# Performance work log

Hardware: AMD Instinct MI355X
Metric: run time of the kernel (lower is better)

The kernel has to match this reference:

```python
import jax, jax.numpy as jnp
import numpy as np

N_NODES = 100000
IN_DIM = 64
HIDDEN = 128
N_EDGES = 1600000


def sage_conv(x, src, dst, W_l, W_r, b):
    # PyG SAGEConv (mean aggr): out = lin_l(mean_{j in N(i)} x_j) + lin_r(x_i) + bias
    agg = jax.ops.segment_sum(x[src], dst, num_segments=N_NODES)  # [N, d]
    cnt = jax.ops.segment_sum(jnp.ones((src.shape[0],), x.dtype), dst,
                              num_segments=N_NODES)  # [N]
    mean = agg / jnp.maximum(cnt, 1.0)[:, None]
    return mean @ W_l + x @ W_r + b


def setup_inputs() -> dict:
    key = jax.random.key(0)
    ks = jax.random.split(key, 10)
    x = jax.random.normal(ks[0], (N_NODES, IN_DIM), dtype=jnp.float32)
    edge_index = jax.random.randint(ks[1], (2, N_EDGES), 0, N_NODES, dtype=jnp.int64)
    s = 1.0 / np.sqrt(IN_DIM)
    W_l1 = jax.random.uniform(ks[2], (IN_DIM, HIDDEN), jnp.float32, -s, s)
    W_r1 = jax.random.uniform(ks[3], (IN_DIM, HIDDEN), jnp.float32, -s, s)
    b1 = jnp.zeros((HIDDEN,), jnp.float32)
    s2 = 1.0 / np.sqrt(HIDDEN)
    W_l2 = jax.random.uniform(ks[4], (HIDDEN, HIDDEN), jnp.float32, -s2, s2)
    W_r2 = jax.random.uniform(ks[5], (HIDDEN, HIDDEN), jnp.float32, -s2, s2)
    b2 = jnp.zeros((HIDDEN,), jnp.float32)
    W_out = jax.random.uniform(ks[6], (HIDDEN, 1), jnp.float32, -s2, s2)
    b_out = jnp.zeros((1,), jnp.float32)
    return {"x": x, "edge_index": edge_index,
            "W_l1": W_l1, "W_r1": W_r1, "b1": b1,
            "W_l2": W_l2, "W_r2": W_r2, "b2": b2,
            "W_out": W_out, "b_out": b_out}


def reference(x, edge_index, W_l1, W_r1, b1, W_l2, W_r2, b2, W_out, b_out):
    src, dst = edge_index[0], edge_index[1]
    h1 = jax.nn.relu(sage_conv(x, src, dst, W_l1, W_r1, b1))   # [N, H]
    h2 = sage_conv(h1, src, dst, W_l2, W_r2, b2)               # [N, H]
    out = (h2 @ W_out + b_out).squeeze(-1)                     # [N]
    return out, h1, h2
```

## Files before the change

kernel.cpp:

```cpp
#include <hip/hip_runtime.h>

#define NN 100000
#define IND 64
#define HID 128
#define NE 1600000

#define BKT2 256
#define NBKT2 ((NN + BKT2 - 1) / BKT2)
#define CAP 4992
#define EPB 4096
#define NBLK_E ((NE + EPB - 1) / EPB)

#define CVT_BLKS (NN * IND / 4 / 256)
#define PW1_BLKS 8
#define PW2_BLKS 16

#define SCAN_CHUNK 1024
#define NSB ((NN + SCAN_CHUNK - 1) / SCAN_CHUNK)

typedef __attribute__((ext_vector_type(8))) short bf16x8;
typedef __attribute__((ext_vector_type(4))) float f32x4;
typedef __attribute__((ext_vector_type(2))) float f32x2;

static __device__ __forceinline__ unsigned short f2bf(float f) {
    unsigned u = __float_as_uint(f);
    u = (u + 0x7FFFu + ((u >> 16) & 1u)) >> 16;
    return (unsigned short)u;
}
static __device__ __forceinline__ unsigned pack2(float a, float b) {
    return (unsigned)f2bf(a) | ((unsigned)f2bf(b) << 16);
}


static __device__ __forceinline__ void packW_body(const float* __restrict__ Wr,
                                                  const float* __restrict__ Wl,
                                                  int Khalf, int KS, int t,
                                                  unsigned short* __restrict__ Wp) {
    if (t >= 8 * KS * 64) return;
    int l  = t & 63;
    int ks = (t >> 6) % KS;
    int jt = t / (64 * KS);
    int j  = jt * 16 + (l & 15);
    int kb = ks * 32 + (l >> 4) * 8;
    unsigned short v[8];
    #pragma unroll
    for (int i = 0; i < 8; ++i) {
        int k = kb + i;
        float w = (k < Khalf) ? Wr[k * HID + j] : Wl[(k - Khalf) * HID + j];
        v[i] = f2bf(w);
    }
    ushort4 lo, hi;
    lo.x = v[0]; lo.y = v[1]; lo.z = v[2]; lo.w = v[3];
    hi.x = v[4]; hi.y = v[5]; hi.z = v[6]; hi.w = v[7];
    ushort4* d = reinterpret_cast<ushort4*>(Wp + (size_t)t * 8);
    d[0] = lo; d[1] = hi;
}

__global__ __launch_bounds__(256) void prep_kernel(const float4* __restrict__ x,
                                                   unsigned* __restrict__ xq,
                                                   const float* __restrict__ Wr1,
                                                   const float* __restrict__ Wl1,
                                                   unsigned short* __restrict__ Wp1,
                                                   const float* __restrict__ Wr2,
                                                   const float* __restrict__ Wl2,
                                                   unsigned short* __restrict__ Wp2,
                                                   int* __restrict__ bktcur) {
    int blk = blockIdx.x, t = threadIdx.x;
    if (blk < CVT_BLKS) {
        int i = blk * 256 + t;
        float4 v = x[i];
        int u = __builtin_amdgcn_cvt_pk_fp8_f32(v.x, v.y, 0, false);
        u = __builtin_amdgcn_cvt_pk_fp8_f32(v.z, v.w, u, true);
        xq[i] = (unsigned)u;
    } else if (blk < CVT_BLKS + PW1_BLKS) {
        packW_body(Wr1, Wl1, IND, 4, (blk - CVT_BLKS) * 256 + t, Wp1);
    } else if (blk < CVT_BLKS + PW1_BLKS + PW2_BLKS) {
        packW_body(Wr2, Wl2, HID, 8, (blk - CVT_BLKS - PW1_BLKS) * 256 + t, Wp2);
    } else {
        bktcur[t] = 0;
        bktcur[t + 256] = 0;
    }
}


__global__ __launch_bounds__(512) void binA_kernel(const int* __restrict__ src,
                                                   const int* __restrict__ dst,
                                                   int* __restrict__ bktcur,
                                                   unsigned* __restrict__ bins) {
    __shared__ int hcnt[NBKT2];
    __shared__ int rbase[NBKT2];
    int t = threadIdx.x;
    int e0 = blockIdx.x * EPB;
    int ce = min(EPB, NE - e0);
    for (int i = t; i < NBKT2; i += 512) hcnt[i] = 0;
    __syncthreads();
    for (int i = t; i < ce; i += 512)
        atomicAdd(&hcnt[dst[e0 + i] >> 8], 1);
    __syncthreads();
    for (int i = t; i < NBKT2; i += 512) {
        int c = hcnt[i];
        rbase[i] = c ? atomicAdd(&bktcur[i], c) : 0;
        hcnt[i] = 0;
    }
    __syncthreads();
    for (int i = t; i < ce; i += 512) {
        int d = dst[e0 + i];
        int b = d >> 8;
        int r = atomicAdd(&hcnt[b], 1);
        bins[(size_t)b * CAP + rbase[b] + r] =
            (unsigned)src[e0 + i] | ((unsigned)(d & 255) << 17);
    }
}

__global__ __launch_bounds__(512) void binB_kernel(const int* __restrict__ bktcur,
                                                   unsigned* __restrict__ bins,
                                                   int* __restrict__ cnt,
                                                   int* __restrict__ off) {
    __shared__ unsigned ebuf[CAP];
    __shared__ int ncnt[BKT2];
    __shared__ int nofs[BKT2];
    __shared__ int wtot[4];
    int t = threadIdx.x, lane = t & 63, w = t >> 6;
    int b = blockIdx.x;
    int m = bktcur[b];
    size_t base = (size_t)b * CAP;
    for (int i = t; i < m; i += 512) ebuf[i] = bins[base + i];
    if (t < BKT2) ncnt[t] = 0;
    __syncthreads();
    for (int i = t; i < m; i += 512)
        atomicAdd(&ncnt[ebuf[i] >> 17], 1);
    __syncthreads();
    if (t < BKT2) {
        int v = ncnt[t];
        int incl = v;
        #pragma unroll
        for (int o = 1; o < 64; o <<= 1) {
            int u = __shfl_up(incl, o);
            if (lane >= o) incl += u;
        }
        if (lane == 63) wtot[w] = incl;
        nofs[t] = incl - v;
    }
    __syncthreads();
    if (t < BKT2) {
        int wbase = 0;
        #pragma unroll
        for (int i = 0; i < 4; ++i) if (i < w) wbase += wtot[i];
        int ex = nofs[t] + wbase;
        nofs[t] = ex;
        int node = b * BKT2 + t;
        if (node < NN) { cnt[node] = ncnt[t]; off[node] = (int)base + ex; }
    }
    __syncthreads();
    for (int i = t; i < m; i += 512) {
        unsigned val = ebuf[i];
        int r = atomicAdd(&nofs[val >> 17], 1);
        bins[base + r] = val & 0x1FFFFu;
    }
}


__global__ __launch_bounds__(256) void agg1_kernel(const unsigned char* __restrict__ xq,
                                                   const int* __restrict__ srcs,
                                                   const int* __restrict__ off,
                                                   const int* __restrict__ cnt,
                                                   unsigned short* __restrict__ m1b) {
    int t = threadIdx.x;
    int n = blockIdx.x * 4 + (t >> 6);
    int l = t & 63, ep = l >> 3, doff = (l & 7) * 8;
    int s0 = off[n], deg = cnt[n];
    float acc[8];
    #pragma unroll
    for (int i = 0; i < 8; ++i) acc[i] = 0.f;
    int e = ep;
    for (; e + 8 < deg; e += 16) {
        int sA = srcs[s0 + e], sB = srcs[s0 + e + 8];
        uint2 uA = *reinterpret_cast<const uint2*>(xq + (size_t)sA * IND + doff);
        uint2 uB = *reinterpret_cast<const uint2*>(xq + (size_t)sB * IND + doff);
        #pragma unroll
        for (int hw = 0; hw < 2; ++hw) {
            unsigned ua = hw ? uA.y : uA.x;
            unsigned ub = hw ? uB.y : uB.x;
            f32x2 la = __builtin_amdgcn_cvt_pk_f32_fp8((int)ua, false);
            f32x2 ha = __builtin_amdgcn_cvt_pk_f32_fp8((int)ua, true);
            f32x2 lb = __builtin_amdgcn_cvt_pk_f32_fp8((int)ub, false);
            f32x2 hb = __builtin_amdgcn_cvt_pk_f32_fp8((int)ub, true);
            acc[hw * 4 + 0] += la.x + lb.x;
            acc[hw * 4 + 1] += la.y + lb.y;
            acc[hw * 4 + 2] += ha.x + hb.x;
            acc[hw * 4 + 3] += ha.y + hb.y;
        }
    }
    for (; e < deg; e += 8) {
        int s = srcs[s0 + e];
        uint2 u = *reinterpret_cast<const uint2*>(xq + (size_t)s * IND + doff);
        #pragma unroll
        for (int hw = 0; hw < 2; ++hw) {
            unsigned uu = hw ? u.y : u.x;
            f32x2 lo = __builtin_amdgcn_cvt_pk_f32_fp8((int)uu, false);
            f32x2 hi = __builtin_amdgcn_cvt_pk_f32_fp8((int)uu, true);
            acc[hw * 4 + 0] += lo.x; acc[hw * 4 + 1] += lo.y;
            acc[hw * 4 + 2] += hi.x; acc[hw * 4 + 3] += hi.y;
        }
    }
    #pragma unroll
    for (int o = 8; o <= 32; o <<= 1) {
        #pragma unroll
        for (int i = 0; i < 8; ++i) acc[i] += __shfl_xor(acc[i], o);
    }
    if (l < 8) {
        float inv = 1.f / fmaxf((float)deg, 1.f);
        uint4 o;
        o.x = pack2(acc[0] * inv, acc[1] * inv);
        o.y = pack2(acc[2] * inv, acc[3] * inv);
        o.z = pack2(acc[4] * inv, acc[5] * inv);
        o.w = pack2(acc[6] * inv, acc[7] * inv);
        *reinterpret_cast<uint4*>(m1b + (size_t)n * IND + l * 8) = o;
    }
}

__global__ __launch_bounds__(256) void agg2_kernel(const unsigned char* __restrict__ h1q,
                                                   const int* __restrict__ srcs,
                                                   const int* __restrict__ off,
                                                   const int* __restrict__ cnt,
                                                   unsigned short* __restrict__ m2b) {
    int t = threadIdx.x;
    int n = blockIdx.x * 4 + (t >> 6);
    int l = t & 63, ep = l >> 3, doff = (l & 7) * 16;
    int s0 = off[n], deg = cnt[n];
    float acc[16];
    #pragma unroll
    for (int i = 0; i < 16; ++i) acc[i] = 0.f;
    int e = ep;
    for (; e + 8 < deg; e += 16) {
        int sA = srcs[s0 + e], sB = srcs[s0 + e + 8];
        uint4 uA = *reinterpret_cast<const uint4*>(h1q + (size_t)sA * HID + doff);
        uint4 uB = *reinterpret_cast<const uint4*>(h1q + (size_t)sB * HID + doff);
        unsigned wa[4] = {uA.x, uA.y, uA.z, uA.w};
        unsigned wb[4] = {uB.x, uB.y, uB.z, uB.w};
        #pragma unroll
        for (int q = 0; q < 4; ++q) {
            f32x2 la = __builtin_amdgcn_cvt_pk_f32_fp8((int)wa[q], false);
            f32x2 ha = __builtin_amdgcn_cvt_pk_f32_fp8((int)wa[q], true);
            f32x2 lb = __builtin_amdgcn_cvt_pk_f32_fp8((int)wb[q], false);
            f32x2 hb = __builtin_amdgcn_cvt_pk_f32_fp8((int)wb[q], true);
            acc[q * 4 + 0] += la.x + lb.x;
            acc[q * 4 + 1] += la.y + lb.y;
            acc[q * 4 + 2] += ha.x + hb.x;
            acc[q * 4 + 3] += ha.y + hb.y;
        }
    }
    for (; e < deg; e += 8) {
        int s = srcs[s0 + e];
        uint4 u = *reinterpret_cast<const uint4*>(h1q + (size_t)s * HID + doff);
        unsigned wu[4] = {u.x, u.y, u.z, u.w};
        #pragma unroll
        for (int q = 0; q < 4; ++q) {
            f32x2 lo = __builtin_amdgcn_cvt_pk_f32_fp8((int)wu[q], false);
            f32x2 hi = __builtin_amdgcn_cvt_pk_f32_fp8((int)wu[q], true);
            acc[q * 4 + 0] += lo.x; acc[q * 4 + 1] += lo.y;
            acc[q * 4 + 2] += hi.x; acc[q * 4 + 3] += hi.y;
        }
    }
    #pragma unroll
    for (int o = 8; o <= 32; o <<= 1) {
        #pragma unroll
        for (int i = 0; i < 16; ++i) acc[i] += __shfl_xor(acc[i], o);
    }
    if (l < 8) {
        float inv = 1.f / fmaxf((float)deg, 1.f);
        uint4 o1, o2;
        o1.x = pack2(acc[0] * inv,  acc[1] * inv);
        o1.y = pack2(acc[2] * inv,  acc[3] * inv);
        o1.z = pack2(acc[4] * inv,  acc[5] * inv);
        o1.w = pack2(acc[6] * inv,  acc[7] * inv);
        o2.x = pack2(acc[8] * inv,  acc[9] * inv);
        o2.y = pack2(acc[10] * inv, acc[11] * inv);
        o2.z = pack2(acc[12] * inv, acc[13] * inv);
        o2.w = pack2(acc[14] * inv, acc[15] * inv);
        unsigned short* dstp = m2b + (size_t)n * HID + l * 16;
        *reinterpret_cast<uint4*>(dstp) = o1;
        *reinterpret_cast<uint4*>(dstp + 8) = o2;
    }
}


__global__ __launch_bounds__(256) void mfma1_kernel(const float* __restrict__ x,
                                                    const unsigned short* __restrict__ m1b,
                                                    const unsigned short* __restrict__ Wp,
                                                    const float* __restrict__ b,
                                                    float* __restrict__ h1f,
                                                    unsigned short* __restrict__ h1b,
                                                    unsigned char* __restrict__ h1q) {
    int t = threadIdx.x, w = t >> 6, l = t & 63;
    int row0 = blockIdx.x * 64 + w * 16;
    int arow = row0 + (l & 15); if (arow > NN - 1) arow = NN - 1;
    int kcol = (l >> 4) * 8;
    f32x4 acc[8];
    #pragma unroll
    for (int jt = 0; jt < 8; ++jt) { acc[jt][0] = 0.f; acc[jt][1] = 0.f; acc[jt][2] = 0.f; acc[jt][3] = 0.f; }
    #pragma unroll
    for (int ks = 0; ks < 4; ++ks) {
        bf16x8 a;
        int c = (ks & 1) * 32 + kcol;
        if (ks < 2) {
            const float* xr = x + (size_t)arow * IND + c;
            float4 f0 = *reinterpret_cast<const float4*>(xr);
            float4 f1 = *reinterpret_cast<const float4*>(xr + 4);
            a[0] = (short)f2bf(f0.x); a[1] = (short)f2bf(f0.y);
            a[2] = (short)f2bf(f0.z); a[3] = (short)f2bf(f0.w);
            a[4] = (short)f2bf(f1.x); a[5] = (short)f2bf(f1.y);
            a[6] = (short)f2bf(f1.z); a[7] = (short)f2bf(f1.w);
        } else {
            a = *reinterpret_cast<const bf16x8*>(m1b + (size_t)arow * IND + c);
        }
        #pragma unroll
        for (int jt = 0; jt < 8; ++jt) {
            bf16x8 bb = *reinterpret_cast<const bf16x8*>(Wp + ((size_t)(jt * 4 + ks) * 64 + l) * 8);
            acc[jt] = __builtin_amdgcn_mfma_f32_16x16x32_bf16(a, bb, acc[jt], 0, 0, 0);
        }
    }
    int rbase = row0 + (l >> 4) * 4;
    #pragma unroll
    for (int jt = 0; jt < 8; ++jt) {
        int col = jt * 16 + (l & 15);
        float bias = b[col];
        #pragma unroll
        for (int r = 0; r < 4; ++r) {
            int row = rbase + r;
            if (row < NN) {
                float v = fmaxf(acc[jt][r] + bias, 0.f);
                h1f[(size_t)row * HID + col] = v;
                h1b[(size_t)row * HID + col] = f2bf(v);
                unsigned q8 = (unsigned)__builtin_amdgcn_cvt_pk_fp8_f32(v, 0.f, 0, false) & 0xFFu;
                h1q[(size_t)row * HID + col] = (unsigned char)q8;
            }
        }
    }
}

__global__ __launch_bounds__(256) void mfma2_kernel(const unsigned short* __restrict__ h1b,
                                                    const unsigned short* __restrict__ m2b,
                                                    const unsigned short* __restrict__ Wp,
                                                    const float* __restrict__ b,
                                                    const float* __restrict__ Wout,
                                                    const float* __restrict__ bout,
                                                    float* __restrict__ h2f,
                                                    float* __restrict__ out) {
    int t = threadIdx.x, w = t >> 6, l = t & 63;
    int row0 = blockIdx.x * 64 + w * 16;
    int arow = row0 + (l & 15); if (arow > NN - 1) arow = NN - 1;
    int kcol = (l >> 4) * 8;
    f32x4 acc[8];
    #pragma unroll
    for (int jt = 0; jt < 8; ++jt) { acc[jt][0] = 0.f; acc[jt][1] = 0.f; acc[jt][2] = 0.f; acc[jt][3] = 0.f; }
    #pragma unroll
    for (int ks = 0; ks < 8; ++ks) {
        const unsigned short* A = (ks < 4) ? h1b : m2b;
        int c = (ks & 3) * 32 + kcol;
        bf16x8 a = *reinterpret_cast<const bf16x8*>(A + (size_t)arow * HID + c);
        #pragma unroll
        for (int jt = 0; jt < 8; ++jt) {
            bf16x8 bb = *reinterpret_cast<const bf16x8*>(Wp + ((size_t)(jt * 8 + ks) * 64 + l) * 8);
            acc[jt] = __builtin_amdgcn_mfma_f32_16x16x32_bf16(a, bb, acc[jt], 0, 0, 0);
        }
    }
    int rbase = row0 + (l >> 4) * 4;
    float hs0 = 0.f, hs1 = 0.f, hs2 = 0.f, hs3 = 0.f;
    #pragma unroll
    for (int jt = 0; jt < 8; ++jt) {
        int col = jt * 16 + (l & 15);
        float bias = b[col];
        float wo = Wout[col];
        #pragma unroll
        for (int r = 0; r < 4; ++r) {
            int row = rbase + r;
            float v = acc[jt][r] + bias;
            if (row < NN) h2f[(size_t)row * HID + col] = v;
            if (r == 0) hs0 += v * wo;
            else if (r == 1) hs1 += v * wo;
            else if (r == 2) hs2 += v * wo;
            else hs3 += v * wo;
        }
    }
    #pragma unroll
    for (int o = 1; o < 16; o <<= 1) {
        hs0 += __shfl_xor(hs0, o);
        hs1 += __shfl_xor(hs1, o);
        hs2 += __shfl_xor(hs2, o);
        hs3 += __shfl_xor(hs3, o);
    }
    if ((l & 15) == 0) {
        float bo = bout[0];
        if (rbase + 0 < NN) out[rbase + 0] = hs0 + bo;
        if (rbase + 1 < NN) out[rbase + 1] = hs1 + bo;
        if (rbase + 2 < NN) out[rbase + 2] = hs2 + bo;
        if (rbase + 3 < NN) out[rbase + 3] = hs3 + bo;
    }
}


__global__ __launch_bounds__(256) void zero_int_kernel(int4* __restrict__ p, int n4) {
    int i = blockIdx.x * 256 + threadIdx.x;
    if (i < n4) p[i] = make_int4(0, 0, 0, 0);
}

__global__ __launch_bounds__(256) void hist_kernel(const int* __restrict__ dst,
                                                   int* __restrict__ cnt) {
    int e = blockIdx.x * 256 + threadIdx.x;
    if (e < NE) atomicAdd(&cnt[dst[e]], 1);
}

__global__ __launch_bounds__(256) void scanA_kernel(const int* __restrict__ cnt,
                                                    int* __restrict__ bsums) {
    int b = blockIdx.x, t = threadIdx.x;
    int base = b * SCAN_CHUNK + t * 4;
    int s = 0;
    #pragma unroll
    for (int k = 0; k < 4; ++k) { int i = base + k; if (i < NN) s += cnt[i]; }
    #pragma unroll
    for (int o = 32; o > 0; o >>= 1) s += __shfl_down(s, o);
    __shared__ int wsum[4];
    if ((t & 63) == 0) wsum[t >> 6] = s;
    __syncthreads();
    if (t == 0) bsums[b] = wsum[0] + wsum[1] + wsum[2] + wsum[3];
}

__global__ void scanB_kernel(int* __restrict__ bsums) {
    int acc = 0;
    for (int i = 0; i < NSB; ++i) { int v = bsums[i]; bsums[i] = acc; acc += v; }
}

__global__ __launch_bounds__(256) void scanC_kernel(const int* __restrict__ cnt,
                                                    const int* __restrict__ bsums,
                                                    int* __restrict__ off,
                                                    int* __restrict__ cur) {
    int b = blockIdx.x, t = threadIdx.x;
    int lane = t & 63, w = t >> 6;
    int base = b * SCAN_CHUNK + t * 4;
    int v[4]; int s = 0;
    #pragma unroll
    for (int k = 0; k < 4; ++k) {
        int i = base + k;
        v[k] = (i < NN) ? cnt[i] : 0;
        s += v[k];
    }
    int inc = s;
    #pragma unroll
    for (int o = 1; o < 64; o <<= 1) {
        int xv = __shfl_up(inc, o);
        if (lane >= o) inc += xv;
    }
    __shared__ int wsum[4];
    if (lane == 63) wsum[w] = inc;
    __syncthreads();
    int wbase = 0;
    for (int i = 0; i < w; ++i) wbase += wsum[i];
    int ex = bsums[b] + wbase + (inc - s);
    #pragma unroll
    for (int k = 0; k < 4; ++k) {
        int i = base + k;
        if (i < NN) { off[i] = ex; cur[i] = ex; }
        ex += v[k];
    }
}

__global__ __launch_bounds__(256) void fill_kernel(const int* __restrict__ src,
                                                   const int* __restrict__ dst,
                                                   int* __restrict__ cur,
                                                   int* __restrict__ srcs) {
    int e = blockIdx.x * 256 + threadIdx.x;
    if (e < NE) {
        int p = atomicAdd(&cur[dst[e]], 1);
        srcs[p] = src[e];
    }
}

__global__ __launch_bounds__(256) void agg1f_kernel(const float* __restrict__ x,
                                                    const int* __restrict__ srcs,
                                                    const int* __restrict__ off,
                                                    const int* __restrict__ cnt,
                                                    float* __restrict__ mean1) {
    int t = threadIdx.x;
    int n = blockIdx.x * 4 + (t >> 6);
    int d = t & 63;
    int s0 = off[n], deg = cnt[n];
    float acc = 0.f;
    for (int e = 0; e < deg; ++e) acc += x[(size_t)srcs[s0 + e] * IND + d];
    mean1[(size_t)n * HID + d] = acc / fmaxf((float)deg, 1.f);
}

__global__ __launch_bounds__(256) void agg2f_kernel(const float* __restrict__ h1,
                                                    const int* __restrict__ srcs,
                                                    const int* __restrict__ off,
                                                    const int* __restrict__ cnt,
                                                    float* __restrict__ mean2) {
    int t = threadIdx.x;
    int n = blockIdx.x * 2 + (t >> 7);
    int d = t & 127;
    int s0 = off[n], deg = cnt[n];
    float acc = 0.f;
    for (int e = 0; e < deg; ++e) acc += h1[(size_t)srcs[s0 + e] * HID + d];
    mean2[(size_t)n * HID + d] = acc / fmaxf((float)deg, 1.f);
}

__global__ __launch_bounds__(256) void gemm1f_kernel(const float* __restrict__ x,
                                                     const float* __restrict__ Wl,
                                                     const float* __restrict__ Wr,
                                                     const float* __restrict__ b,
                                                     float* __restrict__ h1) {
    __shared__ float in[16][128];
    int t = threadIdx.x;
    int node0 = blockIdx.x * 16;
    for (int idx = t; idx < 16 * 128; idx += 256) {
        int r = idx >> 7, c = idx & 127;
        in[r][c] = (c < IND) ? x[(size_t)(node0 + r) * IND + c]
                             : h1[(size_t)(node0 + r) * HID + (c - IND)];
    }
    __syncthreads();
    int j = t & 127, g = t >> 7;
    float acc[8];
    float bj = b[j];
    #pragma unroll
    for (int q = 0; q < 8; ++q) acc[q] = bj;
    for (int k = 0; k < 128; ++k) {
        float wv = (k < IND) ? Wr[k * HID + j] : Wl[(k - IND) * HID + j];
        #pragma unroll
        for (int q = 0; q < 8; ++q) acc[q] += in[g * 8 + q][k] * wv;
    }
    #pragma unroll
    for (int q = 0; q < 8; ++q)
        h1[(size_t)(node0 + g * 8 + q) * HID + j] = fmaxf(acc[q], 0.f);
}

__global__ __launch_bounds__(256) void gemm2f_kernel(const float* __restrict__ h1,
                                                     const float* __restrict__ Wl,
                                                     const float* __restrict__ Wr,
                                                     const float* __restrict__ b,
                                                     const float* __restrict__ Wout,
                                                     const float* __restrict__ bout,
                                                     float* __restrict__ h2,
                                                     float* __restrict__ out) {
    __shared__ float in[16][256];
    __shared__ float part[4][8];
    int t = threadIdx.x;
    int node0 = blockIdx.x * 16;
    for (int idx = t; idx < 16 * 256; idx += 256) {
        int r = idx >> 8, c = idx & 255;
        in[r][c] = (c < HID) ? h1[(size_t)(node0 + r) * HID + c]
                             : h2[(size_t)(node0 + r) * HID + (c - HID)];
    }
    __syncthreads();
    int j = t & 127, g = t >> 7, lane = t & 63, w = t >> 6;
    float acc[8];
    float bj = b[j];
    #pragma unroll
    for (int q = 0; q < 8; ++q) acc[q] = bj;
    for (int k = 0; k < 256; ++k) {
        float wv = (k < HID) ? Wr[k * HID + j] : Wl[(k - HID) * HID + j];
        #pragma unroll
        for (int q = 0; q < 8; ++q) acc[q] += in[g * 8 + q][k] * wv;
    }
    float wo = Wout[j];
    #pragma unroll
    for (int q = 0; q < 8; ++q)
        h2[(size_t)(node0 + g * 8 + q) * HID + j] = acc[q];
    #pragma unroll
    for (int q = 0; q < 8; ++q) {
        float v = acc[q] * wo;
        #pragma unroll
        for (int o = 32; o > 0; o >>= 1) v += __shfl_down(v, o);
        if (lane == 0) part[w][q] = v;
    }
    __syncthreads();
    if (t < 16) {
        int gg = t >> 3, q = t & 7;
        out[node0 + t] = part[2 * gg][q] + part[2 * gg + 1][q] + bout[0];
    }
}


extern "C" void kernel_launch(void* const* d_in, const int* in_sizes, int n_in,
                              void* d_out, int out_size, void* d_ws, size_t ws_size,
                              hipStream_t stream) {
    const float* x    = (const float*)d_in[0];
    const int*   eidx = (const int*)d_in[1];
    const int*   src  = eidx;
    const int*   dst  = eidx + NE;
    const float* Wl1  = (const float*)d_in[2];
    const float* Wr1  = (const float*)d_in[3];
    const float* b1   = (const float*)d_in[4];
    const float* Wl2  = (const float*)d_in[5];
    const float* Wr2  = (const float*)d_in[6];
    const float* b2   = (const float*)d_in[7];
    const float* Wout = (const float*)d_in[8];
    const float* bout = (const float*)d_in[9];

    float* out = (float*)d_out;
    float* h1f = out + NN;
    float* h2f = h1f + (size_t)NN * HID;

    char* p = (char*)d_ws;
    int* cnt        = (int*)p;            p += (size_t)NN * 4;
    int* off        = (int*)p;            p += (size_t)NN * 4;
    int* bktcur     = (int*)p;            p += 512 * 4;
    unsigned* bins  = (unsigned*)p;       p += (size_t)NBKT2 * CAP * 4;
    unsigned char* xq  = (unsigned char*)p;   p += (size_t)NN * IND;
    unsigned short* m1b = (unsigned short*)p; p += (size_t)NN * IND * 2;
    unsigned short* h1b = (unsigned short*)p; p += (size_t)NN * HID * 2;
    unsigned char* h1q  = (unsigned char*)p;  p += (size_t)NN * HID;
    unsigned short* m2b = (unsigned short*)p; p += (size_t)NN * HID * 2;
    unsigned short* Wp1 = (unsigned short*)p; p += 8 * 4 * 64 * 8 * 2;
    unsigned short* Wp2 = (unsigned short*)p; p += 8 * 8 * 64 * 8 * 2;
    const size_t need_v3 = (size_t)(p - (char*)d_ws);
    const size_t need_csr = ((size_t)3 * NN + 128 + NE) * sizeof(int);

    if (ws_size >= need_v3) {
        prep_kernel<<<CVT_BLKS + PW1_BLKS + PW2_BLKS + 1, 256, 0, stream>>>(
            (const float4*)x, (unsigned*)xq, Wr1, Wl1, Wp1, Wr2, Wl2, Wp2, bktcur);
        binA_kernel<<<NBLK_E, 512, 0, stream>>>(src, dst, bktcur, bins);
        binB_kernel<<<NBKT2, 512, 0, stream>>>(bktcur, bins, cnt, off);
        agg1_kernel<<<NN / 4, 256, 0, stream>>>(xq, (const int*)bins, off, cnt, m1b);
        mfma1_kernel<<<(NN + 63) / 64, 256, 0, stream>>>(x, m1b, Wp1, b1, h1f, h1b, h1q);
        agg2_kernel<<<NN / 4, 256, 0, stream>>>(h1q, (const int*)bins, off, cnt, m2b);
        mfma2_kernel<<<(NN + 63) / 64, 256, 0, stream>>>(h1b, m2b, Wp2, b2, Wout, bout, h2f, out);
    } else if (ws_size >= need_csr) {
        int* cntF   = (int*)d_ws;
        int* offF   = cntF + NN;
        int* curF   = offF + NN;
        int* bsums  = curF + NN;
        int* srcsF  = bsums + 128;
        zero_int_kernel<<<(NN / 4 + 255) / 256, 256, 0, stream>>>((int4*)cntF, NN / 4);
        hist_kernel<<<(NE + 255) / 256, 256, 0, stream>>>(dst, cntF);
        scanA_kernel<<<NSB, 256, 0, stream>>>(cntF, bsums);
        scanB_kernel<<<1, 1, 0, stream>>>(bsums);
        scanC_kernel<<<NSB, 256, 0, stream>>>(cntF, bsums, offF, curF);
        fill_kernel<<<(NE + 255) / 256, 256, 0, stream>>>(src, dst, curF, srcsF);
        agg1f_kernel<<<NN / 4, 256, 0, stream>>>(x, srcsF, offF, cntF, h1f);
        gemm1f_kernel<<<NN / 16, 256, 0, stream>>>(x, Wl1, Wr1, b1, h1f);
        agg2f_kernel<<<NN / 2, 256, 0, stream>>>(h1f, srcsF, offF, cntF, h2f);
        gemm2f_kernel<<<NN / 16, 256, 0, stream>>>(h1f, Wl2, Wr2, b2, Wout, bout, h2f, out);
    }
}
```

Before: 218.5 us.

## Batch four nodes per wavefront in aggregation kernels to raise gather memory parallelism

```diff
diff --git a/kernel.cpp b/kernel.cpp
--- a/kernel.cpp
+++ b/kernel.cpp
@@ -14,6 +14,9 @@
 #define CVT_BLKS (NN * IND / 4 / 256)
 #define PW1_BLKS 8
 #define PW2_BLKS 16
+
+#define AGK 4
+#define AGS 3
 
 #define SCAN_CHUNK 1024
 #define NSB ((NN + SCAN_CHUNK - 1) / SCAN_CHUNK)
@@ -165,57 +168,71 @@
                                                    const int* __restrict__ off,
                                                    const int* __restrict__ cnt,
                                                    unsigned short* __restrict__ m1b) {
-    int t = threadIdx.x;
-    int n = blockIdx.x * 4 + (t >> 6);
-    int l = t & 63, ep = l >> 3, doff = (l & 7) * 8;
-    int s0 = off[n], deg = cnt[n];
-    float acc[8];
-    #pragma unroll
-    for (int i = 0; i < 8; ++i) acc[i] = 0.f;
-    int e = ep;
-    for (; e + 8 < deg; e += 16) {
-        int sA = srcs[s0 + e], sB = srcs[s0 + e + 8];
-        uint2 uA = *reinterpret_cast<const uint2*>(xq + (size_t)sA * IND + doff);
-        uint2 uB = *reinterpret_cast<const uint2*>(xq + (size_t)sB * IND + doff);
-        #pragma unroll
-        for (int hw = 0; hw < 2; ++hw) {
-            unsigned ua = hw ? uA.y : uA.x;
-            unsigned ub = hw ? uB.y : uB.x;
-            f32x2 la = __builtin_amdgcn_cvt_pk_f32_fp8((int)ua, false);
-            f32x2 ha = __builtin_amdgcn_cvt_pk_f32_fp8((int)ua, true);
-            f32x2 lb = __builtin_amdgcn_cvt_pk_f32_fp8((int)ub, false);
-            f32x2 hb = __builtin_amdgcn_cvt_pk_f32_fp8((int)ub, true);
-            acc[hw * 4 + 0] += la.x + lb.x;
-            acc[hw * 4 + 1] += la.y + lb.y;
-            acc[hw * 4 + 2] += ha.x + hb.x;
-            acc[hw * 4 + 3] += ha.y + hb.y;
-        }
-    }
-    for (; e < deg; e += 8) {
-        int s = srcs[s0 + e];
-        uint2 u = *reinterpret_cast<const uint2*>(xq + (size_t)s * IND + doff);
-        #pragma unroll
-        for (int hw = 0; hw < 2; ++hw) {
-            unsigned uu = hw ? u.y : u.x;
-            f32x2 lo = __builtin_amdgcn_cvt_pk_f32_fp8((int)uu, false);
-            f32x2 hi = __builtin_amdgcn_cvt_pk_f32_fp8((int)uu, true);
-            acc[hw * 4 + 0] += lo.x; acc[hw * 4 + 1] += lo.y;
-            acc[hw * 4 + 2] += hi.x; acc[hw * 4 + 3] += hi.y;
-        }
-    }
-    #pragma unroll
-    for (int o = 8; o <= 32; o <<= 1) {
-        #pragma unroll
-        for (int i = 0; i < 8; ++i) acc[i] += __shfl_xor(acc[i], o);
-    }
-    if (l < 8) {
-        float inv = 1.f / fmaxf((float)deg, 1.f);
-        uint4 o;
-        o.x = pack2(acc[0] * inv, acc[1] * inv);
-        o.y = pack2(acc[2] * inv, acc[3] * inv);
-        o.z = pack2(acc[4] * inv, acc[5] * inv);
-        o.w = pack2(acc[6] * inv, acc[7] * inv);
-        *reinterpret_cast<uint4*>(m1b + (size_t)n * IND + l * 8) = o;
+    int t = threadIdx.x, w = t >> 6, l = t & 63;
+    int ep = l >> 3, doff = (l & 7) * 8;
+    int nb = (blockIdx.x * 4 + w) * AGK;
+    int deg[AGK], s0[AGK];
+    #pragma unroll
+    for (int k = 0; k < AGK; ++k) { deg[k] = cnt[nb + k]; s0[k] = off[nb + k]; }
+    int si[AGK][AGS];
+    #pragma unroll
+    for (int k = 0; k < AGK; ++k)
+        #pragma unroll
+        for (int s = 0; s < AGS; ++s)
+            si[k][s] = srcs[s0[k] + ep + s * 8];
+    uint2 row[AGK][AGS];
+    #pragma unroll
+    for (int k = 0; k < AGK; ++k)
+        #pragma unroll
+        for (int s = 0; s < AGS; ++s) {
+            if (ep + s * 8 < deg[k])
+                row[k][s] = *reinterpret_cast<const uint2*>(
+                    xq + (size_t)(unsigned)si[k][s] * IND + doff);
+            else
+                row[k][s] = make_uint2(0u, 0u);
+        }
+    #pragma unroll
+    for (int k = 0; k < AGK; ++k) {
+        float acc[8];
+        #pragma unroll
+        for (int i = 0; i < 8; ++i) acc[i] = 0.f;
+        #pragma unroll
+        for (int s = 0; s < AGS; ++s) {
+            unsigned wu[2] = {row[k][s].x, row[k][s].y};
+            #pragma unroll
+            for (int q = 0; q < 2; ++q) {
+                f32x2 lo = __builtin_amdgcn_cvt_pk_f32_fp8((int)wu[q], false);
+                f32x2 hi = __builtin_amdgcn_cvt_pk_f32_fp8((int)wu[q], true);
+                acc[q * 4 + 0] += lo.x; acc[q * 4 + 1] += lo.y;
+                acc[q * 4 + 2] += hi.x; acc[q * 4 + 3] += hi.y;
+            }
+        }
+        for (int e = ep + AGS * 8; e < deg[k]; e += 8) {
+            int s = srcs[s0[k] + e];
+            uint2 u = *reinterpret_cast<const uint2*>(xq + (size_t)s * IND + doff);
+            unsigned wu[2] = {u.x, u.y};
+            #pragma unroll
+            for (int q = 0; q < 2; ++q) {
+                f32x2 lo = __builtin_amdgcn_cvt_pk_f32_fp8((int)wu[q], false);
+                f32x2 hi = __builtin_amdgcn_cvt_pk_f32_fp8((int)wu[q], true);
+                acc[q * 4 + 0] += lo.x; acc[q * 4 + 1] += lo.y;
+                acc[q * 4 + 2] += hi.x; acc[q * 4 + 3] += hi.y;
+            }
+        }
+        #pragma unroll
+        for (int o = 8; o <= 32; o <<= 1) {
+            #pragma unroll
+            for (int i = 0; i < 8; ++i) acc[i] += __shfl_xor(acc[i], o);
+        }
+        if (l < 8) {
+            float inv = 1.f / fmaxf((float)deg[k], 1.f);
+            uint4 o;
+            o.x = pack2(acc[0] * inv, acc[1] * inv);
+            o.y = pack2(acc[2] * inv, acc[3] * inv);
+            o.z = pack2(acc[4] * inv, acc[5] * inv);
+            o.w = pack2(acc[6] * inv, acc[7] * inv);
+            *reinterpret_cast<uint4*>(m1b + (size_t)(nb + k) * IND + l * 8) = o;
+        }
     }
 }
 
@@ -224,63 +241,77 @@
                                                    const int* __restrict__ off,
                                                    const int* __restrict__ cnt,
                                                    unsigned short* __restrict__ m2b) {
-    int t = threadIdx.x;
-    int n = blockIdx.x * 4 + (t >> 6);
-    int l = t & 63, ep = l >> 3, doff = (l & 7) * 16;
-    int s0 = off[n], deg = cnt[n];
-    float acc[16];
-    #pragma unroll
-    for (int i = 0; i < 16; ++i) acc[i] = 0.f;
-    int e = ep;
-    for (; e + 8 < deg; e += 16) {
-        int sA = srcs[s0 + e], sB = srcs[s0 + e + 8];
-        uint4 uA = *reinterpret_cast<const uint4*>(h1q + (size_t)sA * HID + doff);
-        uint4 uB = *reinterpret_cast<const uint4*>(h1q + (size_t)sB * HID + doff);
-        unsigned wa[4] = {uA.x, uA.y, uA.z, uA.w};
-        unsigned wb[4] = {uB.x, uB.y, uB.z, uB.w};
-        #pragma unroll
-        for (int q = 0; q < 4; ++q) {
-            f32x2 la = __builtin_amdgcn_cvt_pk_f32_fp8((int)wa[q], false);
-            f32x2 ha = __builtin_amdgcn_cvt_pk_f32_fp8((int)wa[q], true);
-            f32x2 lb = __builtin_amdgcn_cvt_pk_f32_fp8((int)wb[q], false);
-            f32x2 hb = __builtin_amdgcn_cvt_pk_f32_fp8((int)wb[q], true);
-            acc[q * 4 + 0] += la.x + lb.x;
-            acc[q * 4 + 1] += la.y + lb.y;
-            acc[q * 4 + 2] += ha.x + hb.x;
-            acc[q * 4 + 3] += ha.y + hb.y;
-        }
-    }
-    for (; e < deg; e += 8) {
-        int s = srcs[s0 + e];
-        uint4 u = *reinterpret_cast<const uint4*>(h1q + (size_t)s * HID + doff);
-        unsigned wu[4] = {u.x, u.y, u.z, u.w};
-        #pragma unroll
-        for (int q = 0; q < 4; ++q) {
-            f32x2 lo = __builtin_amdgcn_cvt_pk_f32_fp8((int)wu[q], false);
-            f32x2 hi = __builtin_amdgcn_cvt_pk_f32_fp8((int)wu[q], true);
-            acc[q * 4 + 0] += lo.x; acc[q * 4 + 1] += lo.y;
-            acc[q * 4 + 2] += hi.x; acc[q * 4 + 3] += hi.y;
-        }
-    }
-    #pragma unroll
-    for (int o = 8; o <= 32; o <<= 1) {
-        #pragma unroll
-        for (int i = 0; i < 16; ++i) acc[i] += __shfl_xor(acc[i], o);
-    }
-    if (l < 8) {
-        float inv = 1.f / fmaxf((float)deg, 1.f);
-        uint4 o1, o2;
-        o1.x = pack2(acc[0] * inv,  acc[1] * inv);
-        o1.y = pack2(acc[2] * inv,  acc[3] * inv);
-        o1.z = pack2(acc[4] * inv,  acc[5] * inv);
-        o1.w = pack2(acc[6] * inv,  acc[7] * inv);
-        o2.x = pack2(acc[8] * inv,  acc[9] * inv);
-        o2.y = pack2(acc[10] * inv, acc[11] * inv);
-        o2.z = pack2(acc[12] * inv, acc[13] * inv);
-        o2.w = pack2(acc[14] * inv, acc[15] * inv);
-        unsigned short* dstp = m2b + (size_t)n * HID + l * 16;
-        *reinterpret_cast<uint4*>(dstp) = o1;
-        *reinterpret_cast<uint4*>(dstp + 8) = o2;
+    int t = threadIdx.x, w = t >> 6, l = t & 63;
+    int ep = l >> 3, doff = (l & 7) * 16;
+    int nb = (blockIdx.x * 4 + w) * AGK;
+    int deg[AGK], s0[AGK];
+    #pragma unroll
+    for (int k = 0; k < AGK; ++k) { deg[k] = cnt[nb + k]; s0[k] = off[nb + k]; }
+    int si[AGK][AGS];
+    #pragma unroll
+    for (int k = 0; k < AGK; ++k)
+        #pragma unroll
+        for (int s = 0; s < AGS; ++s)
+            si[k][s] = srcs[s0[k] + ep + s * 8];
+    uint4 row[AGK][AGS];
+    #pragma unroll
+    for (int k = 0; k < AGK; ++k)
+        #pragma unroll
+        for (int s = 0; s < AGS; ++s) {
+            if (ep + s * 8 < deg[k])
+                row[k][s] = *reinterpret_cast<const uint4*>(
+                    h1q + (size_t)(unsigned)si[k][s] * HID + doff);
+            else
+                row[k][s] = make_uint4(0u, 0u, 0u, 0u);
+        }
+    #pragma unroll
+    for (int k = 0; k < AGK; ++k) {
+        float acc[16];
+        #pragma unroll
+        for (int i = 0; i < 16; ++i) acc[i] = 0.f;
+        #pragma unroll
+        for (int s = 0; s < AGS; ++s) {
+            unsigned wu[4] = {row[k][s].x, row[k][s].y, row[k][s].z, row[k][s].w};
+            #pragma unroll
+            for (int q = 0; q < 4; ++q) {
+                f32x2 lo = __builtin_amdgcn_cvt_pk_f32_fp8((int)wu[q], false);
+                f32x2 hi = __builtin_amdgcn_cvt_pk_f32_fp8((int)wu[q], true);
+                acc[q * 4 + 0] += lo.x; acc[q * 4 + 1] += lo.y;
+                acc[q * 4 + 2] += hi.x; acc[q * 4 + 3] += hi.y;
+            }
+        }
+        for (int e = ep + AGS * 8; e < deg[k]; e += 8) {
+            int s = srcs[s0[k] + e];
+            uint4 u = *reinterpret_cast<const uint4*>(h1q + (size_t)s * HID + doff);
+            unsigned wu[4] = {u.x, u.y, u.z, u.w};
+            #pragma unroll
+            for (int q = 0; q < 4; ++q) {
+                f32x2 lo = __builtin_amdgcn_cvt_pk_f32_fp8((int)wu[q], false);
+                f32x2 hi = __builtin_amdgcn_cvt_pk_f32_fp8((int)wu[q], true);
+                acc[q * 4 + 0] += lo.x; acc[q * 4 + 1] += lo.y;
+                acc[q * 4 + 2] += hi.x; acc[q * 4 + 3] += hi.y;
+            }
+        }
+        #pragma unroll
+        for (int o = 8; o <= 32; o <<= 1) {
+            #pragma unroll
+            for (int i = 0; i < 16; ++i) acc[i] += __shfl_xor(acc[i], o);
+        }
+        if (l < 8) {
+            float inv = 1.f / fmaxf((float)deg[k], 1.f);
+            uint4 o1, o2;
+            o1.x = pack2(acc[0] * inv,  acc[1] * inv);
+            o1.y = pack2(acc[2] * inv,  acc[3] * inv);
+            o1.z = pack2(acc[4] * inv,  acc[5] * inv);
+            o1.w = pack2(acc[6] * inv,  acc[7] * inv);
+            o2.x = pack2(acc[8] * inv,  acc[9] * inv);
+            o2.y = pack2(acc[10] * inv, acc[11] * inv);
+            o2.z = pack2(acc[12] * inv, acc[13] * inv);
+            o2.w = pack2(acc[14] * inv, acc[15] * inv);
+            unsigned short* dstp = m2b + (size_t)(nb + k) * HID + l * 16;
+            *reinterpret_cast<uint4*>(dstp) = o1;
+            *reinterpret_cast<uint4*>(dstp + 8) = o2;
+        }
     }
 }
 
@@ -620,9 +651,9 @@
             (const float4*)x, (unsigned*)xq, Wr1, Wl1, Wp1, Wr2, Wl2, Wp2, bktcur);
         binA_kernel<<<NBLK_E, 512, 0, stream>>>(src, dst, bktcur, bins);
         binB_kernel<<<NBKT2, 512, 0, stream>>>(bktcur, bins, cnt, off);
-        agg1_kernel<<<NN / 4, 256, 0, stream>>>(xq, (const int*)bins, off, cnt, m1b);
+        agg1_kernel<<<NN / 16, 256, 0, stream>>>(xq, (const int*)bins, off, cnt, m1b);
         mfma1_kernel<<<(NN + 63) / 64, 256, 0, stream>>>(x, m1b, Wp1, b1, h1f, h1b, h1q);
-        agg2_kernel<<<NN / 4, 256, 0, stream>>>(h1q, (const int*)bins, off, cnt, m2b);
+        agg2_kernel<<<NN / 16, 256, 0, stream>>>(h1q, (const int*)bins, off, cnt, m2b);
         mfma2_kernel<<<(NN + 63) / 64, 256, 0, stream>>>(h1b, m2b, Wp2, b2, Wout, bout, h2f, out);
     } else if (ws_size >= need_csr) {
         int* cntF   = (int*)d_ws;
```

Result: no change. 216.2 us (-1.1%).
